# Optimization experiments

Hardware: AMD Instinct MI355X
Metric: run time of the kernel (lower is better)

Reference implementation:

```python
import jax, jax.numpy as jnp
import numpy as np

N0, N1, N2 = 100000, 40000, 10000
E1, E2 = 640000, 160000
D_IN, D_HID, D_OUT = 256, 256, 128


def segment_mean(msgs, dst, num_segments):
    # PyG mean aggregation: sum of incoming messages / count, 0 for isolated nodes
    s = jax.ops.segment_sum(msgs, dst, num_segments=num_segments)
    cnt = jax.ops.segment_sum(jnp.ones((msgs.shape[0],), msgs.dtype), dst,
                              num_segments=num_segments)
    return s / jnp.maximum(cnt, 1.0)[:, None]


def setup_inputs() -> dict:
    key = jax.random.key(0)
    ks = jax.random.split(key, 10)
    x = jax.random.normal(ks[0], (N0, D_IN), jnp.float32)
    W1l = jax.random.normal(ks[1], (D_IN, D_HID), jnp.float32) * 0.05
    b1 = jnp.zeros((D_HID,), jnp.float32)
    W1r = jax.random.normal(ks[2], (D_IN, D_HID), jnp.float32) * 0.05
    W2l = jax.random.normal(ks[3], (D_HID, D_OUT), jnp.float32) * 0.05
    b2 = jnp.zeros((D_OUT,), jnp.float32)
    W2r = jax.random.normal(ks[4], (D_HID, D_OUT), jnp.float32) * 0.05
    src1 = jax.random.randint(ks[5], (E1,), 0, N0)
    dst1 = jax.random.randint(ks[6], (E1,), 0, N1)
    src2 = jax.random.randint(ks[7], (E2,), 0, N1)
    dst2 = jax.random.randint(ks[8], (E2,), 0, N2)
    return {"x": x, "W1l": W1l, "b1": b1, "W1r": W1r,
            "W2l": W2l, "b2": b2, "W2r": W2r,
            "src1": src1, "dst1": dst1, "src2": src2, "dst2": dst2}


def reference(x, W1l, b1, W1r, W2l, b2, W2r, src1, dst1, src2, dst2):
    # Layer 1: SAGEConv(D_IN -> D_HID) on bipartite (x, x[:N1]) + ReLU
    x_t1 = x[:N1]
    aggr1 = segment_mean(x[src1], dst1, N1)          # [N1, D_IN]
    h = aggr1 @ W1l + b1 + x_t1 @ W1r                # lin_l(aggr)+bias + lin_r(root)
    h = jax.nn.relu(h)
    # Layer 2: SAGEConv(D_HID -> D_OUT) on bipartite (h, h[:N2]) + sigmoid
    x_t2 = h[:N2]
    aggr2 = segment_mean(h[src2], dst2, N2)          # [N2, D_HID]
    out = aggr2 @ W2l + b2 + x_t2 @ W2r
    return jax.nn.sigmoid(out)                       # [N2, D_OUT]
```

## Files before the change

kernel.cpp:

```cpp
#include <hip/hip_runtime.h>
#include <math.h>

#define N0_C  100000
#define N1_C  40000
#define N2_C  10000
#define E1_C  640000
#define E2_C  160000
#define D_IN_C  256
#define D_HID_C 256
#define D_OUT_C 128

#define MAXDEG 128

typedef __attribute__((ext_vector_type(8))) short short8;
typedef __attribute__((ext_vector_type(4))) float float4v;

__device__ __forceinline__ unsigned short f2bf(float f) {
    unsigned int u = __float_as_uint(f);
    return (unsigned short)((u + 0x7FFFu + ((u >> 16) & 1u)) >> 16);
}
__device__ __forceinline__ float bf2f(unsigned int h) {
    return __uint_as_float(h << 16);
}

#define PREP_CONV  6400000
#define PREP_TW    196608
#define PREP_TOTAL (PREP_CONV + PREP_TW + N1_C + N2_C)

__global__ void prep_kernel(const float* __restrict__ x,
                            const float* __restrict__ W1l,
                            const float* __restrict__ W1r,
                            const float* __restrict__ W2l,
                            const float* __restrict__ W2r,
                            unsigned short* __restrict__ xb,
                            unsigned short* __restrict__ wt1l,
                            unsigned short* __restrict__ wt1r,
                            unsigned short* __restrict__ wt2l,
                            unsigned short* __restrict__ wt2r,
                            int* __restrict__ cnt) {
    int stride = gridDim.x * blockDim.x;
    for (int id = blockIdx.x * blockDim.x + threadIdx.x; id < PREP_TOTAL; id += stride) {
        if (id < PREP_CONV) {
            float4 v = ((const float4*)x)[id];
            unsigned long long u = (unsigned long long)f2bf(v.x)
                                 | ((unsigned long long)f2bf(v.y) << 16)
                                 | ((unsigned long long)f2bf(v.z) << 32)
                                 | ((unsigned long long)f2bf(v.w) << 48);
            ((unsigned long long*)xb)[id] = u;
        } else if (id < PREP_CONV + PREP_TW) {
            int t = id - PREP_CONV;
            const float* W; unsigned short* Wt; int N; int off;
            if (t < 65536)       { W = W1l; Wt = wt1l; N = 256; off = t; }
            else if (t < 131072) { W = W1r; Wt = wt1r; N = 256; off = t - 65536; }
            else if (t < 163840) { W = W2l; Wt = wt2l; N = 128; off = t - 131072; }
            else                 { W = W2r; Wt = wt2r; N = 128; off = t - 163840; }
            int k = off / N, n = off - k * N;
            Wt[n * 256 + k] = f2bf(W[off]);
        } else {
            cnt[id - PREP_CONV - PREP_TW] = 0;
        }
    }
}

__global__ void scatter_idx_kernel(const int* __restrict__ src1,
                                   const int* __restrict__ dst1,
                                   const int* __restrict__ src2,
                                   const int* __restrict__ dst2,
                                   int* __restrict__ cnt1, int* __restrict__ cnt2,
                                   int* __restrict__ perm2D1,
                                   int* __restrict__ perm2D2) {
    int e = blockIdx.x * blockDim.x + threadIdx.x;
    if (e < E1_C) {
        int d = min(max(dst1[e], 0), N1_C - 1);
        int pos = atomicAdd(&cnt1[d], 1);
        if (pos < MAXDEG) perm2D1[d * MAXDEG + pos] = src1[e];
    } else if (e < E1_C + E2_C) {
        int e2 = e - E1_C;
        int d = min(max(dst2[e2], 0), N2_C - 1);
        int pos = atomicAdd(&cnt2[d], 1);
        if (pos < MAXDEG) perm2D2[d * MAXDEG + pos] = src2[e2];
    }
}

__global__ __launch_bounds__(256)
void gather_mean_bf16_kernel(const unsigned short* __restrict__ feat,
                             const int* __restrict__ cnt,
                             const int* __restrict__ perm2D,
                             unsigned short* __restrict__ aggr,
                             int n, int nfeat) {
    int node = blockIdx.x * 4 + (threadIdx.x >> 6);
    int lane = threadIdx.x & 63;
    if (node >= n) return;
    const int c_true = cnt[node];
    const int m = min(max(c_true, 0), MAXDEG);
    const int* __restrict__ row = perm2D + (size_t)node * MAXDEG;
    float a0 = 0.f, a1 = 0.f, a2 = 0.f, a3 = 0.f;
    int i = 0;
    for (; i + 4 <= m; i += 4) {
        int s0 = min(max(row[i + 0], 0), nfeat - 1);
        int s1 = min(max(row[i + 1], 0), nfeat - 1);
        int s2 = min(max(row[i + 2], 0), nfeat - 1);
        int s3 = min(max(row[i + 3], 0), nfeat - 1);
        unsigned long long u0 = *(const unsigned long long*)(feat + (size_t)s0 * 256 + lane * 4);
        unsigned long long u1 = *(const unsigned long long*)(feat + (size_t)s1 * 256 + lane * 4);
        unsigned long long u2 = *(const unsigned long long*)(feat + (size_t)s2 * 256 + lane * 4);
        unsigned long long u3 = *(const unsigned long long*)(feat + (size_t)s3 * 256 + lane * 4);
        a0 += bf2f((unsigned int)(u0      ) & 0xFFFFu) + bf2f((unsigned int)(u1      ) & 0xFFFFu)
            + bf2f((unsigned int)(u2      ) & 0xFFFFu) + bf2f((unsigned int)(u3      ) & 0xFFFFu);
        a1 += bf2f((unsigned int)(u0 >> 16) & 0xFFFFu) + bf2f((unsigned int)(u1 >> 16) & 0xFFFFu)
            + bf2f((unsigned int)(u2 >> 16) & 0xFFFFu) + bf2f((unsigned int)(u3 >> 16) & 0xFFFFu);
        a2 += bf2f((unsigned int)(u0 >> 32) & 0xFFFFu) + bf2f((unsigned int)(u1 >> 32) & 0xFFFFu)
            + bf2f((unsigned int)(u2 >> 32) & 0xFFFFu) + bf2f((unsigned int)(u3 >> 32) & 0xFFFFu);
        a3 += bf2f((unsigned int)(u0 >> 48)          ) + bf2f((unsigned int)(u1 >> 48)          )
            + bf2f((unsigned int)(u2 >> 48)          ) + bf2f((unsigned int)(u3 >> 48)          );
    }
    for (; i < m; ++i) {
        int s = min(max(row[i], 0), nfeat - 1);
        unsigned long long u = *(const unsigned long long*)(feat + (size_t)s * 256 + lane * 4);
        a0 += bf2f((unsigned int)(u      ) & 0xFFFFu);
        a1 += bf2f((unsigned int)(u >> 16) & 0xFFFFu);
        a2 += bf2f((unsigned int)(u >> 32) & 0xFFFFu);
        a3 += bf2f((unsigned int)(u >> 48)          );
    }
    float inv = (c_true > 0) ? 1.0f / (float)c_true : 0.0f;
    unsigned long long u = (unsigned long long)f2bf(a0 * inv)
                         | ((unsigned long long)f2bf(a1 * inv) << 16)
                         | ((unsigned long long)f2bf(a2 * inv) << 32)
                         | ((unsigned long long)f2bf(a3 * inv) << 48);
    *(unsigned long long*)(aggr + (size_t)node * 256 + lane * 4) = u;
}

__global__ __launch_bounds__(512)
void mfma_gemm1_kernel(const unsigned short* A0,
                       const unsigned short* A1,
                       const unsigned short* __restrict__ Wt0,
                       const unsigned short* __restrict__ Wt1,
                       const float* __restrict__ bias,
                       unsigned short* out_bf,
                       int M) {
    __shared__ unsigned short As[64][72];
    __shared__ unsigned short Bs[256][72];

    const int tid  = threadIdx.x;
    const int lane = tid & 63;
    const int wid  = tid >> 6;
    const int wm   = wid & 1;
    const int wn   = wid >> 1;
    const int lr   = lane & 15;
    const int kq   = lane >> 4;
    const int row0 = blockIdx.x * 64;

    float4v acc[2][4];
    #pragma unroll
    for (int a = 0; a < 2; ++a)
        #pragma unroll
        for (int b = 0; b < 4; ++b)
            #pragma unroll
            for (int c = 0; c < 4; ++c) acc[a][b][c] = 0.f;

    for (int p = 0; p < 2; ++p) {
        const unsigned short* A  = p ? A1  : A0;
        const unsigned short* __restrict__ Wt = p ? Wt1 : Wt0;
        for (int kt = 0; kt < 4; ++kt) {
            const int k0 = kt * 64;
            __syncthreads();
            {
                int r = tid >> 3, sc = (tid & 7) * 8;
                int row = row0 + r;
                if (row > M - 1) row = M - 1;
                *(short8*)&As[r][sc] = *(const short8*)(A + (size_t)row * 256 + k0 + sc);
            }
            #pragma unroll
            for (int i = 0; i < 4; ++i) {
                int idx = tid + i * 512;
                int r = idx >> 3, sc = (idx & 7) * 8;
                *(short8*)&Bs[r][sc] = *(const short8*)(Wt + (size_t)r * 256 + k0 + sc);
            }
            __syncthreads();
            #pragma unroll
            for (int ks = 0; ks < 64; ks += 32) {
                short8 af[2], bfr[4];
                #pragma unroll
                for (int t = 0; t < 2; ++t)
                    af[t]  = *(const short8*)&As[wm * 32 + t * 16 + lr][ks + kq * 8];
                #pragma unroll
                for (int t = 0; t < 4; ++t)
                    bfr[t] = *(const short8*)&Bs[wn * 64 + t * 16 + lr][ks + kq * 8];
                #pragma unroll
                for (int ar = 0; ar < 2; ++ar)
                    #pragma unroll
                    for (int bc = 0; bc < 4; ++bc)
                        acc[ar][bc] = __builtin_amdgcn_mfma_f32_16x16x32_bf16(
                            af[ar], bfr[bc], acc[ar][bc], 0, 0, 0);
            }
        }
    }

    #pragma unroll
    for (int bc = 0; bc < 4; ++bc) {
        int col = wn * 64 + bc * 16 + lr;
        float bv = bias[col];
        #pragma unroll
        for (int ar = 0; ar < 2; ++ar) {
            int rowb = row0 + wm * 32 + ar * 16 + kq * 4;
            #pragma unroll
            for (int i = 0; i < 4; ++i) {
                int row = rowb + i;
                if (row < M)
                    out_bf[(size_t)row * 256 + col] = f2bf(fmaxf(acc[ar][bc][i] + bv, 0.f));
            }
        }
    }
}

__global__ __launch_bounds__(256)
void mfma_gemm2_kernel(const unsigned short* __restrict__ A0,
                       const unsigned short* __restrict__ A1,
                       const unsigned short* __restrict__ Wt0,
                       const unsigned short* __restrict__ Wt1,
                       const float* __restrict__ bias,
                       float* __restrict__ out_f,
                       int M, int N) {
    __shared__ unsigned short As[64][72];
    __shared__ unsigned short Bs[128][72];

    const int tid  = threadIdx.x;
    const int lane = tid & 63;
    const int wid  = tid >> 6;
    const int wm   = wid & 1;
    const int wn   = wid >> 1;
    const int lr   = lane & 15;
    const int kq   = lane >> 4;
    const int row0 = blockIdx.x * 64;

    float4v acc[2][4];
    #pragma unroll
    for (int a = 0; a < 2; ++a)
        #pragma unroll
        for (int b = 0; b < 4; ++b)
            #pragma unroll
            for (int c = 0; c < 4; ++c) acc[a][b][c] = 0.f;

    for (int p = 0; p < 2; ++p) {
        const unsigned short* __restrict__ A  = p ? A1  : A0;
        const unsigned short* __restrict__ Wt = p ? Wt1 : Wt0;
        for (int kt = 0; kt < 4; ++kt) {
            const int k0 = kt * 64;
            __syncthreads();
            #pragma unroll
            for (int i = 0; i < 2; ++i) {
                int idx = tid + i * 256;
                int r = idx >> 3, sc = (idx & 7) * 8;
                int row = row0 + r;
                if (row > M - 1) row = M - 1;
                *(short8*)&As[r][sc] = *(const short8*)(A + (size_t)row * 256 + k0 + sc);
            }
            #pragma unroll
            for (int i = 0; i < 4; ++i) {
                int idx = tid + i * 256;
                int r = idx >> 3, sc = (idx & 7) * 8;
                *(short8*)&Bs[r][sc] = *(const short8*)(Wt + (size_t)r * 256 + k0 + sc);
            }
            __syncthreads();
            #pragma unroll
            for (int ks = 0; ks < 64; ks += 32) {
                short8 af[2], bfr[4];
                #pragma unroll
                for (int t = 0; t < 2; ++t)
                    af[t]  = *(const short8*)&As[wm * 32 + t * 16 + lr][ks + kq * 8];
                #pragma unroll
                for (int t = 0; t < 4; ++t)
                    bfr[t] = *(const short8*)&Bs[wn * 64 + t * 16 + lr][ks + kq * 8];
                #pragma unroll
                for (int ar = 0; ar < 2; ++ar)
                    #pragma unroll
                    for (int bc = 0; bc < 4; ++bc)
                        acc[ar][bc] = __builtin_amdgcn_mfma_f32_16x16x32_bf16(
                            af[ar], bfr[bc], acc[ar][bc], 0, 0, 0);
            }
        }
    }

    #pragma unroll
    for (int bc = 0; bc < 4; ++bc) {
        int col = wn * 64 + bc * 16 + lr;
        float bv = bias[col];
        #pragma unroll
        for (int ar = 0; ar < 2; ++ar) {
            int rowb = row0 + wm * 32 + ar * 16 + kq * 4;
            #pragma unroll
            for (int i = 0; i < 4; ++i) {
                int row = rowb + i;
                if (row < M)
                    out_f[(size_t)row * N + col] =
                        1.0f / (1.0f + __expf(-(acc[ar][bc][i] + bv)));
            }
        }
    }
}

extern "C" void kernel_launch(void* const* d_in, const int* in_sizes, int n_in,
                              void* d_out, int out_size, void* d_ws, size_t ws_size,
                              hipStream_t stream) {
    const float* x   = (const float*)d_in[0];
    const float* W1l = (const float*)d_in[1];
    const float* b1  = (const float*)d_in[2];
    const float* W1r = (const float*)d_in[3];
    const float* W2l = (const float*)d_in[4];
    const float* b2  = (const float*)d_in[5];
    const float* W2r = (const float*)d_in[6];
    const int* src1  = (const int*)d_in[7];
    const int* dst1  = (const int*)d_in[8];
    const int* src2  = (const int*)d_in[9];
    const int* dst2  = (const int*)d_in[10];
    float* out = (float*)d_out;

    unsigned short* us = (unsigned short*)d_ws;
    unsigned short* xb    = us;                          us += (size_t)N0_C * 256;
    unsigned short* h     = xb;
    unsigned short* aggr1 = us;                          us += (size_t)N1_C * 256;
    unsigned short* aggr2 = aggr1;
    unsigned short* wt1l  = us;                          us += 256 * 256;
    unsigned short* wt1r  = us;                          us += 256 * 256;
    unsigned short* wt2l  = us;                          us += 128 * 256;
    unsigned short* wt2r  = us;                          us += 128 * 256;
    int* ip = (int*)us;
    int* cnt1    = ip;                 ip += N1_C;
    int* cnt2    = ip;                 ip += N2_C;
    int* perm2D1 = ip;                 ip += (size_t)N1_C * MAXDEG;
    int* perm2D2 = ip;                 ip += (size_t)N2_C * MAXDEG;

    prep_kernel<<<2048, 256, 0, stream>>>(x, W1l, W1r, W2l, W2r,
                                          xb, wt1l, wt1r, wt2l, wt2r, cnt1);

    scatter_idx_kernel<<<(E1_C + E2_C + 255) / 256, 256, 0, stream>>>(
        src1, dst1, src2, dst2, cnt1, cnt2, perm2D1, perm2D2);

    gather_mean_bf16_kernel<<<(N1_C + 3) / 4, 256, 0, stream>>>(xb, cnt1, perm2D1,
                                                                aggr1, N1_C, N0_C);
    mfma_gemm1_kernel<<<(N1_C + 63) / 64, 512, 0, stream>>>(aggr1, xb, wt1l, wt1r,
                                                            b1, h, N1_C);

    gather_mean_bf16_kernel<<<(N2_C + 3) / 4, 256, 0, stream>>>(h, cnt2, perm2D2,
                                                                aggr2, N2_C, N1_C);
    mfma_gemm2_kernel<<<(N2_C + 63) / 64, 256, 0, stream>>>(aggr2, h, wt2l, wt2r,
                                                            b2, out, N2_C, D_OUT_C);
}
```

Before: 336.8 us.

## Fuse neighbor mean-gather into both SAGE GEMM kernels via shared-memory aggregate tile

Each GEMM block now first gathers and averages neighbor features for its 64 destination rows straight into a shared-memory tile. The lin_l pass reads the A operand from that tile, so the standalone gather kernels and the global aggr round-trip go away. The layer-1 output h moves to its own buffer instead of aliasing xb, because the fused kernel reads xb while writing h. In exchange, the gather now runs with fewer rows in flight per wave. It is serialized before the MFMA work inside each block and uses more LDS per block, which may reduce occupancy and latency hiding.

```diff
diff --git a/kernel.cpp b/kernel.cpp
--- a/kernel.cpp
+++ b/kernel.cpp
@@ -82,18 +82,9 @@
     }
 }
 
-__global__ __launch_bounds__(256)
-void gather_mean_bf16_kernel(const unsigned short* __restrict__ feat,
-                             const int* __restrict__ cnt,
-                             const int* __restrict__ perm2D,
-                             unsigned short* __restrict__ aggr,
-                             int n, int nfeat) {
-    int node = blockIdx.x * 4 + (threadIdx.x >> 6);
-    int lane = threadIdx.x & 63;
-    if (node >= n) return;
-    const int c_true = cnt[node];
-    const int m = min(max(c_true, 0), MAXDEG);
-    const int* __restrict__ row = perm2D + (size_t)node * MAXDEG;
+__device__ __forceinline__ unsigned long long gather_row_u64(
+        const unsigned short* __restrict__ feat,
+        const int* __restrict__ row, int m, int c_true, int nfeat, int lane) {
     float a0 = 0.f, a1 = 0.f, a2 = 0.f, a3 = 0.f;
     int i = 0;
     for (; i + 4 <= m; i += 4) {
@@ -123,21 +114,22 @@
         a3 += bf2f((unsigned int)(u >> 48)          );
     }
     float inv = (c_true > 0) ? 1.0f / (float)c_true : 0.0f;
-    unsigned long long u = (unsigned long long)f2bf(a0 * inv)
-                         | ((unsigned long long)f2bf(a1 * inv) << 16)
-                         | ((unsigned long long)f2bf(a2 * inv) << 32)
-                         | ((unsigned long long)f2bf(a3 * inv) << 48);
-    *(unsigned long long*)(aggr + (size_t)node * 256 + lane * 4) = u;
+    return (unsigned long long)f2bf(a0 * inv)
+         | ((unsigned long long)f2bf(a1 * inv) << 16)
+         | ((unsigned long long)f2bf(a2 * inv) << 32)
+         | ((unsigned long long)f2bf(a3 * inv) << 48);
 }
 
 __global__ __launch_bounds__(512)
-void mfma_gemm1_kernel(const unsigned short* A0,
-                       const unsigned short* A1,
-                       const unsigned short* __restrict__ Wt0,
-                       const unsigned short* __restrict__ Wt1,
-                       const float* __restrict__ bias,
-                       unsigned short* out_bf,
-                       int M) {
+void fused_gather_gemm1_kernel(const unsigned short* __restrict__ feat,
+                               const int* __restrict__ cnt,
+                               const int* __restrict__ perm2D,
+                               const unsigned short* __restrict__ Wt0,
+                               const unsigned short* __restrict__ Wt1,
+                               const float* __restrict__ bias,
+                               unsigned short* __restrict__ out_bf,
+                               int M, int nfeat) {
+    __shared__ unsigned short Af[64][264];
     __shared__ unsigned short As[64][72];
     __shared__ unsigned short Bs[256][72];
 
@@ -150,6 +142,20 @@
     const int kq   = lane >> 4;
     const int row0 = blockIdx.x * 64;
 
+    #pragma unroll 1
+    for (int j = 0; j < 8; ++j) {
+        int r = wid * 8 + j;
+        int node = row0 + r;
+        unsigned long long u = 0ull;
+        if (node < M) {
+            const int c_true = cnt[node];
+            const int m = min(max(c_true, 0), MAXDEG);
+            const int* __restrict__ prow = perm2D + (size_t)node * MAXDEG;
+            u = gather_row_u64(feat, prow, m, c_true, nfeat, lane);
+        }
+        *(unsigned long long*)&Af[r][lane * 4] = u;
+    }
+
     float4v acc[2][4];
     #pragma unroll
     for (int a = 0; a < 2; ++a)
@@ -159,16 +165,15 @@
             for (int c = 0; c < 4; ++c) acc[a][b][c] = 0.f;
 
     for (int p = 0; p < 2; ++p) {
-        const unsigned short* A  = p ? A1  : A0;
         const unsigned short* __restrict__ Wt = p ? Wt1 : Wt0;
         for (int kt = 0; kt < 4; ++kt) {
             const int k0 = kt * 64;
             __syncthreads();
-            {
+            if (p) {
                 int r = tid >> 3, sc = (tid & 7) * 8;
                 int row = row0 + r;
                 if (row > M - 1) row = M - 1;
-                *(short8*)&As[r][sc] = *(const short8*)(A + (size_t)row * 256 + k0 + sc);
+                *(short8*)&As[r][sc] = *(const short8*)(feat + (size_t)row * 256 + k0 + sc);
             }
             #pragma unroll
             for (int i = 0; i < 4; ++i) {
@@ -180,9 +185,15 @@
             #pragma unroll
             for (int ks = 0; ks < 64; ks += 32) {
                 short8 af[2], bfr[4];
-                #pragma unroll
-                for (int t = 0; t < 2; ++t)
-                    af[t]  = *(const short8*)&As[wm * 32 + t * 16 + lr][ks + kq * 8];
+                if (p == 0) {
+                    #pragma unroll
+                    for (int t = 0; t < 2; ++t)
+                        af[t]  = *(const short8*)&Af[wm * 32 + t * 16 + lr][k0 + ks + kq * 8];
+                } else {
+                    #pragma unroll
+                    for (int t = 0; t < 2; ++t)
+                        af[t]  = *(const short8*)&As[wm * 32 + t * 16 + lr][ks + kq * 8];
+                }
                 #pragma unroll
                 for (int t = 0; t < 4; ++t)
                     bfr[t] = *(const short8*)&Bs[wn * 64 + t * 16 + lr][ks + kq * 8];
@@ -214,13 +225,15 @@
 }
 
 __global__ __launch_bounds__(256)
-void mfma_gemm2_kernel(const unsigned short* __restrict__ A0,
-                       const unsigned short* __restrict__ A1,
-                       const unsigned short* __restrict__ Wt0,
-                       const unsigned short* __restrict__ Wt1,
-                       const float* __restrict__ bias,
-                       float* __restrict__ out_f,
-                       int M, int N) {
+void fused_gather_gemm2_kernel(const unsigned short* __restrict__ feat,
+                               const int* __restrict__ cnt,
+                               const int* __restrict__ perm2D,
+                               const unsigned short* __restrict__ Wt0,
+                               const unsigned short* __restrict__ Wt1,
+                               const float* __restrict__ bias,
+                               float* __restrict__ out_f,
+                               int M, int N, int nfeat) {
+    __shared__ unsigned short Af[64][264];
     __shared__ unsigned short As[64][72];
     __shared__ unsigned short Bs[128][72];
 
@@ -233,6 +246,20 @@
     const int kq   = lane >> 4;
     const int row0 = blockIdx.x * 64;
 
+    #pragma unroll 1
+    for (int j = 0; j < 16; ++j) {
+        int r = wid * 16 + j;
+        int node = row0 + r;
+        unsigned long long u = 0ull;
+        if (node < M) {
+            const int c_true = cnt[node];
+            const int m = min(max(c_true, 0), MAXDEG);
+            const int* __restrict__ prow = perm2D + (size_t)node * MAXDEG;
+            u = gather_row_u64(feat, prow, m, c_true, nfeat, lane);
+        }
+        *(unsigned long long*)&Af[r][lane * 4] = u;
+    }
+
     float4v acc[2][4];
     #pragma unroll
     for (int a = 0; a < 2; ++a)
@@ -242,18 +269,19 @@
             for (int c = 0; c < 4; ++c) acc[a][b][c] = 0.f;
 
     for (int p = 0; p < 2; ++p) {
-        const unsigned short* __restrict__ A  = p ? A1  : A0;
         const unsigned short* __restrict__ Wt = p ? Wt1 : Wt0;
         for (int kt = 0; kt < 4; ++kt) {
             const int k0 = kt * 64;
             __syncthreads();
-            #pragma unroll
-            for (int i = 0; i < 2; ++i) {
-                int idx = tid + i * 256;
-                int r = idx >> 3, sc = (idx & 7) * 8;
-                int row = row0 + r;
-                if (row > M - 1) row = M - 1;
-                *(short8*)&As[r][sc] = *(const short8*)(A + (size_t)row * 256 + k0 + sc);
+            if (p) {
+                #pragma unroll
+                for (int i = 0; i < 2; ++i) {
+                    int idx = tid + i * 256;
+                    int r = idx >> 3, sc = (idx & 7) * 8;
+                    int row = row0 + r;
+                    if (row > M - 1) row = M - 1;
+                    *(short8*)&As[r][sc] = *(const short8*)(feat + (size_t)row * 256 + k0 + sc);
+                }
             }
             #pragma unroll
             for (int i = 0; i < 4; ++i) {
@@ -265,9 +293,15 @@
             #pragma unroll
             for (int ks = 0; ks < 64; ks += 32) {
                 short8 af[2], bfr[4];
-                #pragma unroll
-                for (int t = 0; t < 2; ++t)
-                    af[t]  = *(const short8*)&As[wm * 32 + t * 16 + lr][ks + kq * 8];
+                if (p == 0) {
+                    #pragma unroll
+                    for (int t = 0; t < 2; ++t)
+                        af[t]  = *(const short8*)&Af[wm * 32 + t * 16 + lr][k0 + ks + kq * 8];
+                } else {
+                    #pragma unroll
+                    for (int t = 0; t < 2; ++t)
+                        af[t]  = *(const short8*)&As[wm * 32 + t * 16 + lr][ks + kq * 8];
+                }
                 #pragma unroll
                 for (int t = 0; t < 4; ++t)
                     bfr[t] = *(const short8*)&Bs[wn * 64 + t * 16 + lr][ks + kq * 8];
@@ -317,9 +351,7 @@
 
     unsigned short* us = (unsigned short*)d_ws;
     unsigned short* xb    = us;                          us += (size_t)N0_C * 256;
-    unsigned short* h     = xb;
-    unsigned short* aggr1 = us;                          us += (size_t)N1_C * 256;
-    unsigned short* aggr2 = aggr1;
+    unsigned short* h     = us;                          us += (size_t)N1_C * 256;
     unsigned short* wt1l  = us;                          us += 256 * 256;
     unsigned short* wt1r  = us;                          us += 256 * 256;
     unsigned short* wt2l  = us;                          us += 128 * 256;
@@ -336,13 +368,9 @@
     scatter_idx_kernel<<<(E1_C + E2_C + 255) / 256, 256, 0, stream>>>(
         src1, dst1, src2, dst2, cnt1, cnt2, perm2D1, perm2D2);
 
-    gather_mean_bf16_kernel<<<(N1_C + 3) / 4, 256, 0, stream>>>(xb, cnt1, perm2D1,
-                                                                aggr1, N1_C, N0_C);
-    mfma_gemm1_kernel<<<(N1_C + 63) / 64, 512, 0, stream>>>(aggr1, xb, wt1l, wt1r,
-                                                            b1, h, N1_C);
-
-    gather_mean_bf16_kernel<<<(N2_C + 3) / 4, 256, 0, stream>>>(h, cnt2, perm2D2,
-                                                                aggr2, N2_C, N1_C);
-    mfma_gemm2_kernel<<<(N2_C + 63) / 64, 256, 0, stream>>>(aggr2, h, wt2l, wt2r,
-                                                            b2, out, N2_C, D_OUT_C);
-}
+    fused_gather_gemm1_kernel<<<(N1_C + 63) / 64, 512, 0, stream>>>(
+        xb, cnt1, perm2D1, wt1l, wt1r, b1, h, N1_C, N0_C);
+
+    fused_gather_gemm2_kernel<<<(N2_C + 63) / 64, 256, 0, stream>>>(
+        h, cnt2, perm2D2, wt2l, wt2r, b2, out, N2_C, D_OUT_C, N1_C);
+}
```

Result: slower. 415.3 us (+23.3%).

## Replace LDS-staged GEMMs with direct-from-global MFMA fragment loads

Applied to the files above, without the earlier changes.

Both SAGE linear-layer GEMMs drop shared-memory staging and __syncthreads, and each wave loads its MFMA fragments straight from global memory. Each wave now computes a 64x64 tile with a 4x4 accumulator grid. GEMM1 uses 256 threads and drops its row bounds checks, relying on N1 being divisible by 64. h and aggr2 move to separate workspace buffers so they no longer alias xb and aggr1, which uses more workspace. Skipping LDS removes barrier stalls and LDS traffic, at the cost of redundant global/L2 reads across waves and strided short8 loads.

```diff
diff --git a/kernel.cpp b/kernel.cpp
--- a/kernel.cpp
+++ b/kernel.cpp
@@ -130,69 +130,52 @@
     *(unsigned long long*)(aggr + (size_t)node * 256 + lane * 4) = u;
 }
 
-__global__ __launch_bounds__(512)
-void mfma_gemm1_kernel(const unsigned short* A0,
-                       const unsigned short* A1,
-                       const unsigned short* __restrict__ Wt0,
-                       const unsigned short* __restrict__ Wt1,
-                       const float* __restrict__ bias,
-                       unsigned short* out_bf,
-                       int M) {
-    __shared__ unsigned short As[64][72];
-    __shared__ unsigned short Bs[256][72];
-
+__global__ __launch_bounds__(256)
+void gemm1_direct_kernel(const unsigned short* __restrict__ A0,
+                         const unsigned short* __restrict__ A1,
+                         const unsigned short* __restrict__ Wt0,
+                         const unsigned short* __restrict__ Wt1,
+                         const float* __restrict__ bias,
+                         unsigned short* __restrict__ out_bf) {
     const int tid  = threadIdx.x;
     const int lane = tid & 63;
-    const int wid  = tid >> 6;
-    const int wm   = wid & 1;
-    const int wn   = wid >> 1;
+    const int wn   = tid >> 6;
     const int lr   = lane & 15;
     const int kq   = lane >> 4;
     const int row0 = blockIdx.x * 64;
 
-    float4v acc[2][4];
+    float4v acc[4][4];
     #pragma unroll
-    for (int a = 0; a < 2; ++a)
+    for (int a = 0; a < 4; ++a)
         #pragma unroll
         for (int b = 0; b < 4; ++b)
             #pragma unroll
             for (int c = 0; c < 4; ++c) acc[a][b][c] = 0.f;
 
+    #pragma unroll 1
     for (int p = 0; p < 2; ++p) {
-        const unsigned short* A  = p ? A1  : A0;
+        const unsigned short* __restrict__ A  = p ? A1  : A0;
         const unsigned short* __restrict__ Wt = p ? Wt1 : Wt0;
-        for (int kt = 0; kt < 4; ++kt) {
-            const int k0 = kt * 64;
-            __syncthreads();
-            {
-                int r = tid >> 3, sc = (tid & 7) * 8;
-                int row = row0 + r;
-                if (row > M - 1) row = M - 1;
-                *(short8*)&As[r][sc] = *(const short8*)(A + (size_t)row * 256 + k0 + sc);
-            }
-            #pragma unroll
-            for (int i = 0; i < 4; ++i) {
-                int idx = tid + i * 512;
-                int r = idx >> 3, sc = (idx & 7) * 8;
-                *(short8*)&Bs[r][sc] = *(const short8*)(Wt + (size_t)r * 256 + k0 + sc);
-            }
-            __syncthreads();
-            #pragma unroll
-            for (int ks = 0; ks < 64; ks += 32) {
-                short8 af[2], bfr[4];
+        const unsigned short* pA[4];
+        const unsigned short* pB[4];
+        #pragma unroll
+        for (int t = 0; t < 4; ++t) {
+            pA[t] = A  + (size_t)(row0 + t * 16 + lr) * 256 + kq * 8;
+            pB[t] = Wt + (size_t)(wn * 64 + t * 16 + lr) * 256 + kq * 8;
+        }
+        #pragma unroll
+        for (int k = 0; k < 256; k += 32) {
+            short8 af[4], bfr[4];
+            #pragma unroll
+            for (int t = 0; t < 4; ++t) af[t]  = *(const short8*)(pA[t] + k);
+            #pragma unroll
+            for (int t = 0; t < 4; ++t) bfr[t] = *(const short8*)(pB[t] + k);
+            #pragma unroll
+            for (int ar = 0; ar < 4; ++ar)
                 #pragma unroll
-                for (int t = 0; t < 2; ++t)
-                    af[t]  = *(const short8*)&As[wm * 32 + t * 16 + lr][ks + kq * 8];
-                #pragma unroll
-                for (int t = 0; t < 4; ++t)
-                    bfr[t] = *(const short8*)&Bs[wn * 64 + t * 16 + lr][ks + kq * 8];
-                #pragma unroll
-                for (int ar = 0; ar < 2; ++ar)
-                    #pragma unroll
-                    for (int bc = 0; bc < 4; ++bc)
-                        acc[ar][bc] = __builtin_amdgcn_mfma_f32_16x16x32_bf16(
-                            af[ar], bfr[bc], acc[ar][bc], 0, 0, 0);
-            }
+                for (int bc = 0; bc < 4; ++bc)
+                    acc[ar][bc] = __builtin_amdgcn_mfma_f32_16x16x32_bf16(
+                        af[ar], bfr[bc], acc[ar][bc], 0, 0, 0);
         }
     }
 
@@ -201,83 +184,68 @@
         int col = wn * 64 + bc * 16 + lr;
         float bv = bias[col];
         #pragma unroll
-        for (int ar = 0; ar < 2; ++ar) {
-            int rowb = row0 + wm * 32 + ar * 16 + kq * 4;
+        for (int ar = 0; ar < 4; ++ar) {
+            int rowb = row0 + ar * 16 + kq * 4;
             #pragma unroll
             for (int i = 0; i < 4; ++i) {
                 int row = rowb + i;
-                if (row < M)
-                    out_bf[(size_t)row * 256 + col] = f2bf(fmaxf(acc[ar][bc][i] + bv, 0.f));
+                out_bf[(size_t)row * 256 + col] = f2bf(fmaxf(acc[ar][bc][i] + bv, 0.f));
             }
         }
     }
 }
 
 __global__ __launch_bounds__(256)
-void mfma_gemm2_kernel(const unsigned short* __restrict__ A0,
-                       const unsigned short* __restrict__ A1,
-                       const unsigned short* __restrict__ Wt0,
-                       const unsigned short* __restrict__ Wt1,
-                       const float* __restrict__ bias,
-                       float* __restrict__ out_f,
-                       int M, int N) {
-    __shared__ unsigned short As[64][72];
-    __shared__ unsigned short Bs[128][72];
-
+void gemm2_direct_kernel(const unsigned short* __restrict__ A0,
+                         const unsigned short* __restrict__ A1,
+                         const unsigned short* __restrict__ Wt0,
+                         const unsigned short* __restrict__ Wt1,
+                         const float* __restrict__ bias,
+                         float* __restrict__ out_f,
+                         int M, int N) {
     const int tid  = threadIdx.x;
     const int lane = tid & 63;
     const int wid  = tid >> 6;
-    const int wm   = wid & 1;
-    const int wn   = wid >> 1;
+    const int wr   = wid >> 1;
+    const int wn   = wid & 1;
     const int lr   = lane & 15;
     const int kq   = lane >> 4;
-    const int row0 = blockIdx.x * 64;
-
-    float4v acc[2][4];
+    const int row0 = blockIdx.x * 128 + wr * 64;
+
+    float4v acc[4][4];
     #pragma unroll
-    for (int a = 0; a < 2; ++a)
+    for (int a = 0; a < 4; ++a)
         #pragma unroll
         for (int b = 0; b < 4; ++b)
             #pragma unroll
             for (int c = 0; c < 4; ++c) acc[a][b][c] = 0.f;
 
+    #pragma unroll 1
     for (int p = 0; p < 2; ++p) {
         const unsigned short* __restrict__ A  = p ? A1  : A0;
         const unsigned short* __restrict__ Wt = p ? Wt1 : Wt0;
-        for (int kt = 0; kt < 4; ++kt) {
-            const int k0 = kt * 64;
-            __syncthreads();
-            #pragma unroll
-            for (int i = 0; i < 2; ++i) {
-                int idx = tid + i * 256;
-                int r = idx >> 3, sc = (idx & 7) * 8;
-                int row = row0 + r;
-                if (row > M - 1) row = M - 1;
-                *(short8*)&As[r][sc] = *(const short8*)(A + (size_t)row * 256 + k0 + sc);
-            }
-            #pragma unroll
-            for (int i = 0; i < 4; ++i) {
-                int idx = tid + i * 256;
-                int r = idx >> 3, sc = (idx & 7) * 8;
-                *(short8*)&Bs[r][sc] = *(const short8*)(Wt + (size_t)r * 256 + k0 + sc);
-            }
-            __syncthreads();
-            #pragma unroll
-            for (int ks = 0; ks < 64; ks += 32) {
-                short8 af[2], bfr[4];
+        const unsigned short* pA[4];
+        const unsigned short* pB[4];
+        #pragma unroll
+        for (int t = 0; t < 4; ++t) {
+            int row = row0 + t * 16 + lr;
+            if (row > M - 1) row = M - 1;
+            pA[t] = A  + (size_t)row * 256 + kq * 8;
+            pB[t] = Wt + (size_t)(wn * 64 + t * 16 + lr) * 256 + kq * 8;
+        }
+        #pragma unroll
+        for (int k = 0; k < 256; k += 32) {
+            short8 af[4], bfr[4];
+            #pragma unroll
+            for (int t = 0; t < 4; ++t) af[t]  = *(const short8*)(pA[t] + k);
+            #pragma unroll
+            for (int t = 0; t < 4; ++t) bfr[t] = *(const short8*)(pB[t] + k);
+            #pragma unroll
+            for (int ar = 0; ar < 4; ++ar)
                 #pragma unroll
-                for (int t = 0; t < 2; ++t)
-                    af[t]  = *(const short8*)&As[wm * 32 + t * 16 + lr][ks + kq * 8];
-                #pragma unroll
-                for (int t = 0; t < 4; ++t)
-                    bfr[t] = *(const short8*)&Bs[wn * 64 + t * 16 + lr][ks + kq * 8];
-                #pragma unroll
-                for (int ar = 0; ar < 2; ++ar)
-                    #pragma unroll
-                    for (int bc = 0; bc < 4; ++bc)
-                        acc[ar][bc] = __builtin_amdgcn_mfma_f32_16x16x32_bf16(
-                            af[ar], bfr[bc], acc[ar][bc], 0, 0, 0);
-            }
+                for (int bc = 0; bc < 4; ++bc)
+                    acc[ar][bc] = __builtin_amdgcn_mfma_f32_16x16x32_bf16(
+                        af[ar], bfr[bc], acc[ar][bc], 0, 0, 0);
         }
     }
 
@@ -286,8 +254,8 @@
         int col = wn * 64 + bc * 16 + lr;
         float bv = bias[col];
         #pragma unroll
-        for (int ar = 0; ar < 2; ++ar) {
-            int rowb = row0 + wm * 32 + ar * 16 + kq * 4;
+        for (int ar = 0; ar < 4; ++ar) {
+            int rowb = row0 + ar * 16 + kq * 4;
             #pragma unroll
             for (int i = 0; i < 4; ++i) {
                 int row = rowb + i;
@@ -317,9 +285,9 @@
 
     unsigned short* us = (unsigned short*)d_ws;
     unsigned short* xb    = us;                          us += (size_t)N0_C * 256;
-    unsigned short* h     = xb;
     unsigned short* aggr1 = us;                          us += (size_t)N1_C * 256;
-    unsigned short* aggr2 = aggr1;
+    unsigned short* h     = us;                          us += (size_t)N1_C * 256;
+    unsigned short* aggr2 = us;                          us += (size_t)N2_C * 256;
     unsigned short* wt1l  = us;                          us += 256 * 256;
     unsigned short* wt1r  = us;                          us += 256 * 256;
     unsigned short* wt2l  = us;                          us += 128 * 256;
@@ -338,11 +306,12 @@
 
     gather_mean_bf16_kernel<<<(N1_C + 3) / 4, 256, 0, stream>>>(xb, cnt1, perm2D1,
                                                                 aggr1, N1_C, N0_C);
-    mfma_gemm1_kernel<<<(N1_C + 63) / 64, 512, 0, stream>>>(aggr1, xb, wt1l, wt1r,
-                                                            b1, h, N1_C);
+
+    gemm1_direct_kernel<<<N1_C / 64, 256, 0, stream>>>(aggr1, xb, wt1l, wt1r, b1, h);
 
     gather_mean_bf16_kernel<<<(N2_C + 3) / 4, 256, 0, stream>>>(h, cnt2, perm2D2,
                                                                 aggr2, N2_C, N1_C);
-    mfma_gemm2_kernel<<<(N2_C + 63) / 64, 256, 0, stream>>>(aggr2, h, wt2l, wt2r,
-                                                            b2, out, N2_C, D_OUT_C);
-}
+
+    gemm2_direct_kernel<<<(N2_C + 127) / 128, 256, 0, stream>>>(
+        aggr2, h, wt2l, wt2r, b2, out, N2_C, D_OUT_C);
+}
```

Result: slower. 378.4 us (+12.4%).
